# Optimization experiments

Hardware: AMD Instinct MI355X
Metric: run time of the kernel (lower is better)

Reference implementation:

```python
import jax, jax.numpy as jnp
import numpy as np

N_NODES = 50000
N_EDGES = 640000
HID = 128
EDGE_FEAT = 4
NUM_G = 20
R_MIN, R_MAX = 0.0, 10.0

def setup_inputs() -> dict:
    key = jax.random.key(0)
    ks = jax.random.split(key, 16)
    s = lambda d: 1.0 / np.sqrt(d)
    return {
        'h': jax.random.normal(ks[0], (N_NODES, HID), jnp.float32),
        'x': jax.random.normal(ks[1], (N_NODES, 3), jnp.float32),
        'edge_index': jax.random.randint(ks[2], (2, N_EDGES), 0, N_NODES, dtype=jnp.int64),
        'mask_ligand': jnp.ones((N_NODES,), jnp.float32),
        'edge_attr': jax.random.normal(ks[3], (N_EDGES, EDGE_FEAT), jnp.float32),
        'We1': jax.random.normal(ks[4], (2*HID+EDGE_FEAT+NUM_G, HID), jnp.float32) * s(2*HID+EDGE_FEAT+NUM_G),
        'be1': jnp.zeros((HID,), jnp.float32),
        'We2': jax.random.normal(ks[5], (HID, HID), jnp.float32) * s(HID),
        'be2': jnp.zeros((HID,), jnp.float32),
        'Winf': jax.random.normal(ks[6], (HID, 1), jnp.float32) * s(HID),
        'binf': jnp.zeros((1,), jnp.float32),
        'Wx1': jax.random.normal(ks[7], (HID, HID), jnp.float32) * s(HID),
        'bx1': jnp.zeros((HID,), jnp.float32),
        'Wx2': jax.random.normal(ks[8], (HID, 1), jnp.float32) * 0.001 * s(HID),
        'Wn1': jax.random.normal(ks[9], (2*HID, HID), jnp.float32) * s(2*HID),
        'bn1': jnp.zeros((HID,), jnp.float32),
        'Wn2': jax.random.normal(ks[10], (HID, HID), jnp.float32) * s(HID),
        'bn2': jnp.zeros((HID,), jnp.float32),
    }

def reference(h, x, edge_index, mask_ligand, edge_attr,
              We1, be1, We2, be2, Winf, binf, Wx1, bx1, Wx2, Wn1, bn1, Wn2, bn2):
    n = h.shape[0]
    src, dst = edge_index[0], edge_index[1]
    hi, hj = h[dst], h[src]                      # [E, H] gathers
    rel_x = x[dst] - x[src]                      # [E, 3]
    d_sq = jnp.sum(rel_x**2, axis=-1, keepdims=True)  # [E, 1]
    d = jnp.sqrt(d_sq + 1e-8)
    # GaussianSmearing(r_min=0, r_max=10, num_gaussians=20)
    offset = jnp.linspace(R_MIN, R_MAX, NUM_G, dtype=h.dtype)
    coeff = -0.5 / (offset[1] - offset[0])**2
    d_feat = jnp.exp(coeff * (d - offset)**2)    # [E, 20]
    edge_feat = jnp.concatenate([d_feat, edge_attr], axis=-1)
    # edge MLP (2 layers, silu, act_last=True)
    z = jnp.concatenate([hi, hj, edge_feat], axis=-1)
    mij = jax.nn.silu(jax.nn.silu(z @ We1 + be1) @ We2 + be2)  # [E, H]
    eij = jax.nn.sigmoid(mij @ Winf + binf)      # [E, 1]
    mi = jax.ops.segment_sum(mij * eij, dst, num_segments=n)   # [N, H]
    # node MLP (2 layers, silu, no act on last)
    nz = jnp.concatenate([mi, h], axis=-1)
    h_out = h + (jax.nn.silu(nz @ Wn1 + bn1) @ Wn2 + bn2)
    # coordinate update
    xg = jnp.tanh(jax.nn.silu(mij @ Wx1 + bx1) @ Wx2)          # [E, 1]
    delta_x = jax.ops.segment_sum(rel_x / (d + 1.0) * xg, dst, num_segments=n)
    x_out = x + delta_x * mask_ligand[:, None]
    return h_out, x_out
```

## Files before the change

### kernel.cpp

```cpp
#include <hip/hip_runtime.h>
#include <math.h>

#define NN 50000
#define NE 640000
#define H 128
#define EPB 32
#define NPB 32
#define ZB 296
#define BB 136
#define KP1 288
#define NZB 264

typedef __attribute__((ext_vector_type(8))) unsigned short u16x8;
typedef __attribute__((ext_vector_type(8))) __bf16 bf16x8;
typedef __attribute__((ext_vector_type(2))) __bf16 bf16x2;
typedef __attribute__((ext_vector_type(4))) float f32x4;

__device__ __forceinline__ float frcp(float x) {
#if __has_builtin(__builtin_amdgcn_rcpf)
    return __builtin_amdgcn_rcpf(x);
#else
    return 1.0f / x;
#endif
}

__device__ __forceinline__ float silu_f(float v) {
    return v * frcp(1.0f + __expf(-v));
}

__device__ __forceinline__ float sigmoid_f(float v) {
    return frcp(1.0f + __expf(-v));
}

__device__ __forceinline__ float tanh_f(float v) {
    return 1.0f - 2.0f * frcp(1.0f + __expf(2.0f * v));
}

__device__ __forceinline__ unsigned short f2bf(float f) {
    unsigned int u = __builtin_bit_cast(unsigned int, f);
    u += 0x7FFFu + ((u >> 16) & 1u);
    return (unsigned short)(u >> 16);
}

__device__ __forceinline__ float bf2f(unsigned short s) {
    unsigned int u = ((unsigned int)s) << 16;
    return __builtin_bit_cast(float, u);
}

__device__ __forceinline__ unsigned int pkbf(float lo, float hi) {
#if __has_builtin(__builtin_amdgcn_cvt_pk_bf16_f32)
    bf16x2 v = __builtin_amdgcn_cvt_pk_bf16_f32(lo, hi);
    unsigned int r; __builtin_memcpy(&r, &v, 4); return r;
#else
    return (unsigned int)f2bf(lo) | ((unsigned int)f2bf(hi) << 16);
#endif
}

__device__ __forceinline__ f32x4 mfma16(u16x8 a, u16x8 b, f32x4 c) {
    return __builtin_amdgcn_mfma_f32_16x16x32_bf16(
        __builtin_bit_cast(bf16x8, a), __builtin_bit_cast(bf16x8, b), c, 0, 0, 0);
}

template<int KT, int INSTR, bool SYNC_BEFORE_EPI>
__device__ __forceinline__ void layer_mfma(
    const unsigned short* __restrict__ inbuf,
    const unsigned short* __restrict__ wt,
    const float* __restrict__ bias,
    unsigned short* __restrict__ outbuf,
    int wv, int quad, int r16)
{
    f32x4 acc[2][2] = {};
    const int F = wv * 32;
    #pragma unroll
    for (int ks = 0; ks < KT / 32; ks++) {
        int ko = ks * 32 + quad * 8;
        u16x8 b0 = *(const u16x8*)(inbuf + r16 * INSTR + ko);
        u16x8 b1 = *(const u16x8*)(inbuf + (16 + r16) * INSTR + ko);
        u16x8 a0 = *(const u16x8*)(wt + (size_t)(F + r16) * KT + ko);
        u16x8 a1 = *(const u16x8*)(wt + (size_t)(F + 16 + r16) * KT + ko);
        acc[0][0] = mfma16(a0, b0, acc[0][0]);
        acc[0][1] = mfma16(a0, b1, acc[0][1]);
        acc[1][0] = mfma16(a1, b0, acc[1][0]);
        acc[1][1] = mfma16(a1, b1, acc[1][1]);
    }
    if (SYNC_BEFORE_EPI) __syncthreads();
    #pragma unroll
    for (int rt = 0; rt < 2; rt++) {
        int f0 = F + rt * 16 + quad * 4;
        float4 bv = *(const float4*)(bias + f0);
        #pragma unroll
        for (int ci = 0; ci < 2; ci++) {
            int e = ci * 16 + r16;
            float s0 = silu_f(acc[rt][ci][0] + bv.x);
            float s1 = silu_f(acc[rt][ci][1] + bv.y);
            float s2 = silu_f(acc[rt][ci][2] + bv.z);
            float s3 = silu_f(acc[rt][ci][3] + bv.w);
            uint2 p = { pkbf(s0, s1), pkbf(s2, s3) };
            *(uint2*)(outbuf + e * BB + f0) = p;
        }
    }
}

__global__ __launch_bounds__(256) void convert_weights(
    const float* __restrict__ We1, const float* __restrict__ We2,
    const float* __restrict__ Wx1, const float* __restrict__ Wn1,
    const float* __restrict__ Wn2,
    unsigned short* __restrict__ w1t, unsigned short* __restrict__ w2t,
    unsigned short* __restrict__ wx1t, unsigned short* __restrict__ wn1t,
    unsigned short* __restrict__ wn2t)
{
    int i = blockIdx.x * 256 + threadIdx.x;
    const int S1 = 128 * KP1;
    const int S2 = 128 * 128;
    const int S3 = 128 * 256;
    if (i < S1) {
        int n = i / KP1, k = i % KP1;
        w1t[i] = (k < 280) ? f2bf(We1[k * H + n]) : (unsigned short)0;
    } else if (i < S1 + S2) {
        int j = i - S1; int n = j / H, k = j % H;
        w2t[j] = f2bf(We2[k * H + n]);
    } else if (i < S1 + 2 * S2) {
        int j = i - S1 - S2; int n = j / H, k = j % H;
        wx1t[j] = f2bf(Wx1[k * H + n]);
    } else if (i < S1 + 2 * S2 + S3) {
        int j = i - S1 - 2 * S2; int n = j / 256, k = j % 256;
        wn1t[j] = f2bf(Wn1[k * H + n]);
    } else if (i < S1 + 3 * S2 + S3) {
        int j = i - S1 - 2 * S2 - S3; int n = j / H, k = j % H;
        wn2t[j] = f2bf(Wn2[k * H + n]);
    }
}

__global__ __launch_bounds__(256) void zero_kernel(float4* __restrict__ p, int n4) {
    int i = blockIdx.x * 256 + threadIdx.x;
    if (i < n4) p[i] = make_float4(0.f, 0.f, 0.f, 0.f);
}

__global__ __launch_bounds__(256, 7) void edge_kernel(
    const float* __restrict__ h, const float* __restrict__ x,
    const int* __restrict__ ei, const float* __restrict__ edge_attr,
    const unsigned short* __restrict__ w1t, const float* __restrict__ be1,
    const unsigned short* __restrict__ w2t, const float* __restrict__ be2,
    const float* __restrict__ Winf, const float* __restrict__ binf,
    const unsigned short* __restrict__ wx1t, const float* __restrict__ bx1,
    const float* __restrict__ Wx2,
    float* __restrict__ mi, float* __restrict__ dx)
{
    __shared__ unsigned short zs[EPB * ZB];
    __shared__ float relx_s[EPB][3];
    __shared__ float eij_s[EPB];
    __shared__ float epart[4][EPB];
    __shared__ float xpart[4][EPB];
    __shared__ int dst_s[EPB];
    __shared__ float winf_s[H];
    __shared__ float wx2_s[H];

    unsigned short* m1 = zs;
    unsigned short* m2 = zs + EPB * BB;

    const int t = threadIdx.x;
    const int e0 = blockIdx.x * EPB;

    if (t >= 128 && t < 256) {
        winf_s[t - 128] = Winf[t - 128];
        wx2_s[t - 128] = Wx2[t - 128];
    }

    {
        int e = t >> 3, l = t & 7;
        int s = ei[e0 + e], d = ei[NE + e0 + e];
        const float4* hd = (const float4*)(h + (size_t)d * H);
        const float4* hs = (const float4*)(h + (size_t)s * H);
        unsigned short* zr = zs + e * ZB;
        float4 v0 = hd[l * 4 + 0], v1 = hd[l * 4 + 1];
        float4 v2 = hd[l * 4 + 2], v3 = hd[l * 4 + 3];
        uint4 p0 = { pkbf(v0.x, v0.y), pkbf(v0.z, v0.w), pkbf(v1.x, v1.y), pkbf(v1.z, v1.w) };
        uint4 p1 = { pkbf(v2.x, v2.y), pkbf(v2.z, v2.w), pkbf(v3.x, v3.y), pkbf(v3.z, v3.w) };
        *(uint4*)(zr + l * 16) = p0;
        *(uint4*)(zr + l * 16 + 8) = p1;
        float4 w0 = hs[l * 4 + 0], w1 = hs[l * 4 + 1];
        float4 w2 = hs[l * 4 + 2], w3 = hs[l * 4 + 3];
        uint4 q0 = { pkbf(w0.x, w0.y), pkbf(w0.z, w0.w), pkbf(w1.x, w1.y), pkbf(w1.z, w1.w) };
        uint4 q1 = { pkbf(w2.x, w2.y), pkbf(w2.z, w2.w), pkbf(w3.x, w3.y), pkbf(w3.z, w3.w) };
        *(uint4*)(zr + 128 + l * 16) = q0;
        *(uint4*)(zr + 128 + l * 16 + 8) = q1;
    }
    if (t < EPB) {
        int s = ei[e0 + t], d = ei[NE + e0 + t];
        dst_s[t] = d;
        float rx = x[d * 3 + 0] - x[s * 3 + 0];
        float ry = x[d * 3 + 1] - x[s * 3 + 1];
        float rz = x[d * 3 + 2] - x[s * 3 + 2];
        float d2 = rx * rx + ry * ry + rz * rz;
        float dd = sqrtf(d2 + 1e-8f);
        float inv = frcp(dd + 1.0f);
        relx_s[t][0] = rx * inv;
        relx_s[t][1] = ry * inv;
        relx_s[t][2] = rz * inv;
        const float step = 10.0f / 19.0f;
        const float coeff = -0.5f / (step * step);
        unsigned short* zr = zs + t * ZB;
        #pragma unroll
        for (int g = 0; g < 20; g++) {
            float df = dd - step * (float)g;
            zr[256 + g] = f2bf(__expf(coeff * df * df));
        }
        #pragma unroll
        for (int j = 0; j < 4; j++)
            zr[276 + j] = f2bf(edge_attr[(size_t)(e0 + t) * 4 + j]);
        #pragma unroll
        for (int j = 280; j < ZB; j++) zr[j] = 0;
    }
    __syncthreads();

    const int wv = t >> 6, lane = t & 63;
    const int quad = lane >> 4, r16 = lane & 15;
    const int F = wv * 32;

    layer_mfma<KP1, ZB, true>(zs, w1t, be1, m1, wv, quad, r16);
    __syncthreads();

    {
        f32x4 acc[2][2] = {};
        #pragma unroll
        for (int ks = 0; ks < H / 32; ks++) {
            int ko = ks * 32 + quad * 8;
            u16x8 b0 = *(const u16x8*)(m1 + r16 * BB + ko);
            u16x8 b1 = *(const u16x8*)(m1 + (16 + r16) * BB + ko);
            u16x8 a0 = *(const u16x8*)(w2t + (size_t)(F + r16) * H + ko);
            u16x8 a1 = *(const u16x8*)(w2t + (size_t)(F + 16 + r16) * H + ko);
            acc[0][0] = mfma16(a0, b0, acc[0][0]);
            acc[0][1] = mfma16(a0, b1, acc[0][1]);
            acc[1][0] = mfma16(a1, b0, acc[1][0]);
            acc[1][1] = mfma16(a1, b1, acc[1][1]);
        }
        float ep[2] = {0.f, 0.f};
        #pragma unroll
        for (int rt = 0; rt < 2; rt++) {
            int f0 = F + rt * 16 + quad * 4;
            float4 bv = *(const float4*)(be2 + f0);
            float4 wf = *(const float4*)(winf_s + f0);
            #pragma unroll
            for (int ci = 0; ci < 2; ci++) {
                int e = ci * 16 + r16;
                float s0 = silu_f(acc[rt][ci][0] + bv.x);
                float s1 = silu_f(acc[rt][ci][1] + bv.y);
                float s2 = silu_f(acc[rt][ci][2] + bv.z);
                float s3 = silu_f(acc[rt][ci][3] + bv.w);
                ep[ci] += s0 * wf.x + s1 * wf.y + s2 * wf.z + s3 * wf.w;
                uint2 p = { pkbf(s0, s1), pkbf(s2, s3) };
                *(uint2*)(m2 + e * BB + f0) = p;
            }
        }
        #pragma unroll
        for (int ci = 0; ci < 2; ci++) {
            ep[ci] += __shfl_xor(ep[ci], 16, 64);
            ep[ci] += __shfl_xor(ep[ci], 32, 64);
        }
        if (quad == 0) {
            epart[wv][r16] = ep[0];
            epart[wv][16 + r16] = ep[1];
        }
    }
    __syncthreads();

    if (t < EPB) {
        float s = epart[0][t] + epart[1][t] + epart[2][t] + epart[3][t] + binf[0];
        eij_s[t] = sigmoid_f(s);
    }

    {
        f32x4 acc[2][2] = {};
        #pragma unroll
        for (int ks = 0; ks < H / 32; ks++) {
            int ko = ks * 32 + quad * 8;
            u16x8 b0 = *(const u16x8*)(m2 + r16 * BB + ko);
            u16x8 b1 = *(const u16x8*)(m2 + (16 + r16) * BB + ko);
            u16x8 a0 = *(const u16x8*)(wx1t + (size_t)(F + r16) * H + ko);
            u16x8 a1 = *(const u16x8*)(wx1t + (size_t)(F + 16 + r16) * H + ko);
            acc[0][0] = mfma16(a0, b0, acc[0][0]);
            acc[0][1] = mfma16(a0, b1, acc[0][1]);
            acc[1][0] = mfma16(a1, b0, acc[1][0]);
            acc[1][1] = mfma16(a1, b1, acc[1][1]);
        }
        float xp[2] = {0.f, 0.f};
        #pragma unroll
        for (int rt = 0; rt < 2; rt++) {
            int f0 = F + rt * 16 + quad * 4;
            float4 bv = *(const float4*)(bx1 + f0);
            float4 wf = *(const float4*)(wx2_s + f0);
            #pragma unroll
            for (int ci = 0; ci < 2; ci++) {
                xp[ci] += silu_f(acc[rt][ci][0] + bv.x) * wf.x
                        + silu_f(acc[rt][ci][1] + bv.y) * wf.y
                        + silu_f(acc[rt][ci][2] + bv.z) * wf.z
                        + silu_f(acc[rt][ci][3] + bv.w) * wf.w;
            }
        }
        #pragma unroll
        for (int ci = 0; ci < 2; ci++) {
            xp[ci] += __shfl_xor(xp[ci], 16, 64);
            xp[ci] += __shfl_xor(xp[ci], 32, 64);
        }
        if (quad == 0) {
            xpart[wv][r16] = xp[0];
            xpart[wv][16 + r16] = xp[1];
        }
    }
    __syncthreads();

    {
        int k = t & 127, eh = t >> 7;
        for (int e = eh; e < EPB; e += 2) {
            float mv = bf2f(m2[e * BB + k]) * eij_s[e];
            atomicAdd(&mi[(size_t)dst_s[e] * H + k], mv);
        }
        if (t < EPB * 3) {
            int e = t / 3, dim = t % 3;
            float xs = xpart[0][e] + xpart[1][e] + xpart[2][e] + xpart[3][e];
            float xg = tanh_f(xs);
            atomicAdd(&dx[(size_t)dst_s[e] * 3 + dim], relx_s[e][dim] * xg);
        }
    }
}

__global__ __launch_bounds__(256, 8) void node_kernel(
    const float* __restrict__ h, const float* __restrict__ x,
    const float* __restrict__ mask,
    const unsigned short* __restrict__ wn1t, const float* __restrict__ bn1,
    const unsigned short* __restrict__ wn2t, const float* __restrict__ bn2,
    float* __restrict__ mi_hout, float* __restrict__ dx_xout)
{
    __shared__ unsigned short nzs[NPB * NZB];

    unsigned short* nbuf = nzs;

    const int t = threadIdx.x;
    const int n0 = blockIdx.x * NPB;

    {
        int r = t >> 3, l = t & 7;
        int n = n0 + r;
        unsigned short* zr = nzs + r * NZB;
        if (n < NN) {
            const float4* mi4 = (const float4*)(mi_hout + (size_t)n * H);
            const float4* h4  = (const float4*)(h + (size_t)n * H);
            float4 v0 = mi4[l * 4 + 0], v1 = mi4[l * 4 + 1];
            float4 v2 = mi4[l * 4 + 2], v3 = mi4[l * 4 + 3];
            uint4 p0 = { pkbf(v0.x, v0.y), pkbf(v0.z, v0.w), pkbf(v1.x, v1.y), pkbf(v1.z, v1.w) };
            uint4 p1 = { pkbf(v2.x, v2.y), pkbf(v2.z, v2.w), pkbf(v3.x, v3.y), pkbf(v3.z, v3.w) };
            *(uint4*)(zr + l * 16) = p0;
            *(uint4*)(zr + l * 16 + 8) = p1;
            float4 w0 = h4[l * 4 + 0], w1 = h4[l * 4 + 1];
            float4 w2 = h4[l * 4 + 2], w3 = h4[l * 4 + 3];
            uint4 q0 = { pkbf(w0.x, w0.y), pkbf(w0.z, w0.w), pkbf(w1.x, w1.y), pkbf(w1.z, w1.w) };
            uint4 q1 = { pkbf(w2.x, w2.y), pkbf(w2.z, w2.w), pkbf(w3.x, w3.y), pkbf(w3.z, w3.w) };
            *(uint4*)(zr + 128 + l * 16) = q0;
            *(uint4*)(zr + 128 + l * 16 + 8) = q1;
        } else {
            uint4 zf = {0u, 0u, 0u, 0u};
            *(uint4*)(zr + l * 16) = zf;
            *(uint4*)(zr + l * 16 + 8) = zf;
            *(uint4*)(zr + 128 + l * 16) = zf;
            *(uint4*)(zr + 128 + l * 16 + 8) = zf;
        }
    }

    float xo = 0.f;
    int xn = -1, xdim = 0;
    if (t < NPB * 3) {
        int r = t / 3; xdim = t % 3;
        int n = n0 + r;
        if (n < NN) {
            xn = n;
            xo = x[(size_t)n * 3 + xdim] + dx_xout[(size_t)n * 3 + xdim] * mask[n];
        }
    }
    __syncthreads();

    if (xn >= 0) dx_xout[(size_t)xn * 3 + xdim] = xo;

    const int wv = t >> 6, lane = t & 63;
    const int quad = lane >> 4, r16 = lane & 15;

    layer_mfma<2 * H, NZB, true>(nzs, wn1t, bn1, nbuf, wv, quad, r16);
    __syncthreads();

    {
        f32x4 acc[2][2] = {};
        const int F = wv * 32;
        #pragma unroll
        for (int ks = 0; ks < H / 32; ks++) {
            int ko = ks * 32 + quad * 8;
            u16x8 b0 = *(const u16x8*)(nbuf + r16 * BB + ko);
            u16x8 b1 = *(const u16x8*)(nbuf + (16 + r16) * BB + ko);
            u16x8 a0 = *(const u16x8*)(wn2t + (size_t)(F + r16) * H + ko);
            u16x8 a1 = *(const u16x8*)(wn2t + (size_t)(F + 16 + r16) * H + ko);
            acc[0][0] = mfma16(a0, b0, acc[0][0]);
            acc[0][1] = mfma16(a0, b1, acc[0][1]);
            acc[1][0] = mfma16(a1, b0, acc[1][0]);
            acc[1][1] = mfma16(a1, b1, acc[1][1]);
        }
        #pragma unroll
        for (int rt = 0; rt < 2; rt++) {
            int f0 = F + rt * 16 + quad * 4;
            float4 bv = *(const float4*)(bn2 + f0);
            #pragma unroll
            for (int ci = 0; ci < 2; ci++) {
                int n = n0 + ci * 16 + r16;
                if (n < NN) {
                    float4 hv = *(const float4*)(h + (size_t)n * H + f0);
                    float4 o;
                    o.x = hv.x + acc[rt][ci][0] + bv.x;
                    o.y = hv.y + acc[rt][ci][1] + bv.y;
                    o.z = hv.z + acc[rt][ci][2] + bv.z;
                    o.w = hv.w + acc[rt][ci][3] + bv.w;
                    *(float4*)(mi_hout + (size_t)n * H + f0) = o;
                }
            }
        }
    }
}

extern "C" void kernel_launch(void* const* d_in, const int* in_sizes, int n_in,
                              void* d_out, int out_size, void* d_ws, size_t ws_size,
                              hipStream_t stream) {
    const float* h     = (const float*)d_in[0];
    const float* x     = (const float*)d_in[1];
    const int*   ei    = (const int*)d_in[2];
    const float* mask  = (const float*)d_in[3];
    const float* eattr = (const float*)d_in[4];
    const float* We1   = (const float*)d_in[5];
    const float* be1   = (const float*)d_in[6];
    const float* We2   = (const float*)d_in[7];
    const float* be2   = (const float*)d_in[8];
    const float* Winf  = (const float*)d_in[9];
    const float* binf  = (const float*)d_in[10];
    const float* Wx1   = (const float*)d_in[11];
    const float* bx1   = (const float*)d_in[12];
    const float* Wx2   = (const float*)d_in[13];
    const float* Wn1   = (const float*)d_in[14];
    const float* bn1   = (const float*)d_in[15];
    const float* Wn2   = (const float*)d_in[16];
    const float* bn2   = (const float*)d_in[17];

    float* mi = (float*)d_out;
    float* dx = mi + (size_t)NN * H;

    unsigned short* w1t  = (unsigned short*)d_ws;
    unsigned short* w2t  = w1t + 128 * KP1;
    unsigned short* wx1t = w2t + 128 * H;
    unsigned short* wn1t = wx1t + 128 * H;
    unsigned short* wn2t = wn1t + 128 * 256;

    const int wconv_total = 128 * KP1 + 3 * 128 * H + 128 * 256;
    convert_weights<<<(wconv_total + 255) / 256, 256, 0, stream>>>(
        We1, We2, Wx1, Wn1, Wn2, w1t, w2t, wx1t, wn1t, wn2t);

    const int total4 = (NN * H + NN * 3) / 4;
    zero_kernel<<<(total4 + 255) / 256, 256, 0, stream>>>((float4*)d_out, total4);

    edge_kernel<<<NE / EPB, 256, 0, stream>>>(
        h, x, ei, eattr, w1t, be1, w2t, be2, Winf, binf, wx1t, bx1, Wx2, mi, dx);

    node_kernel<<<(NN + NPB - 1) / NPB, 256, 0, stream>>>(
        h, x, mask, wn1t, bn1, wn2t, bn2, mi, dx);
}
```

Measured before the change: 525.9 us.

## Sort edges by destination via counting sort and segment-reduce before atomics

After: 558.6 us. 6.2% more time.

```diff
diff --git a/kernel.cpp b/kernel.cpp
--- a/kernel.cpp
+++ b/kernel.cpp
@@ -10,6 +10,7 @@
 #define BB 136
 #define KP1 288
 #define NZB 264
+#define NBPAD 50176
 
 typedef __attribute__((ext_vector_type(8))) unsigned short u16x8;
 typedef __attribute__((ext_vector_type(8))) __bf16 bf16x8;
@@ -136,6 +137,48 @@
     if (i < n4) p[i] = make_float4(0.f, 0.f, 0.f, 0.f);
 }
 
+__global__ __launch_bounds__(256) void hist_kernel(
+    const int* __restrict__ ei, int* __restrict__ cnt)
+{
+    int i = blockIdx.x * 256 + threadIdx.x;
+    if (i < NE) atomicAdd(&cnt[ei[NE + i]], 1);
+}
+
+__global__ __launch_bounds__(256) void scan_kernel(
+    const int* __restrict__ cnt, int* __restrict__ cur)
+{
+    __shared__ int part[256];
+    const int t = threadIdx.x;
+    const int lo = t * (NBPAD / 256);
+    int s = 0;
+    for (int i = 0; i < NBPAD / 256; i++) s += cnt[lo + i];
+    part[t] = s;
+    __syncthreads();
+    #pragma unroll
+    for (int d = 1; d < 256; d <<= 1) {
+        int v = (t >= d) ? part[t - d] : 0;
+        __syncthreads();
+        part[t] += v;
+        __syncthreads();
+    }
+    int run = (t > 0) ? part[t - 1] : 0;
+    for (int i = 0; i < NBPAD / 256; i++) {
+        cur[lo + i] = run;
+        run += cnt[lo + i];
+    }
+}
+
+__global__ __launch_bounds__(256) void scatter_kernel(
+    const int* __restrict__ ei, int* __restrict__ cur, int* __restrict__ perm)
+{
+    int i = blockIdx.x * 256 + threadIdx.x;
+    if (i < NE) {
+        int d = ei[NE + i];
+        int p = atomicAdd(&cur[d], 1);
+        perm[p] = i;
+    }
+}
+
 __global__ __launch_bounds__(256, 7) void edge_kernel(
     const float* __restrict__ h, const float* __restrict__ x,
     const int* __restrict__ ei, const float* __restrict__ edge_attr,
@@ -143,7 +186,7 @@
     const unsigned short* __restrict__ w2t, const float* __restrict__ be2,
     const float* __restrict__ Winf, const float* __restrict__ binf,
     const unsigned short* __restrict__ wx1t, const float* __restrict__ bx1,
-    const float* __restrict__ Wx2,
+    const float* __restrict__ Wx2, const int* __restrict__ perm,
     float* __restrict__ mi, float* __restrict__ dx)
 {
     __shared__ unsigned short zs[EPB * ZB];
@@ -160,6 +203,7 @@
 
     const int t = threadIdx.x;
     const int e0 = blockIdx.x * EPB;
+    const bool srt = (perm != nullptr);
 
     if (t >= 128 && t < 256) {
         winf_s[t - 128] = Winf[t - 128];
@@ -168,7 +212,8 @@
 
     {
         int e = t >> 3, l = t & 7;
-        int s = ei[e0 + e], d = ei[NE + e0 + e];
+        int ep = srt ? perm[e0 + e] : (e0 + e);
+        int s = ei[ep], d = ei[NE + ep];
         const float4* hd = (const float4*)(h + (size_t)d * H);
         const float4* hs = (const float4*)(h + (size_t)s * H);
         unsigned short* zr = zs + e * ZB;
@@ -186,7 +231,8 @@
         *(uint4*)(zr + 128 + l * 16 + 8) = q1;
     }
     if (t < EPB) {
-        int s = ei[e0 + t], d = ei[NE + e0 + t];
+        int ep = srt ? perm[e0 + t] : (e0 + t);
+        int s = ei[ep], d = ei[NE + ep];
         dst_s[t] = d;
         float rx = x[d * 3 + 0] - x[s * 3 + 0];
         float ry = x[d * 3 + 1] - x[s * 3 + 1];
@@ -207,7 +253,7 @@
         }
         #pragma unroll
         for (int j = 0; j < 4; j++)
-            zr[276 + j] = f2bf(edge_attr[(size_t)(e0 + t) * 4 + j]);
+            zr[276 + j] = f2bf(edge_attr[(size_t)ep * 4 + j]);
         #pragma unroll
         for (int j = 280; j < ZB; j++) zr[j] = 0;
     }
@@ -310,16 +356,33 @@
     __syncthreads();
 
     {
-        int k = t & 127, eh = t >> 7;
-        for (int e = eh; e < EPB; e += 2) {
-            float mv = bf2f(m2[e * BB + k]) * eij_s[e];
-            atomicAdd(&mi[(size_t)dst_s[e] * H + k], mv);
-        }
-        if (t < EPB * 3) {
-            int e = t / 3, dim = t % 3;
-            float xs = xpart[0][e] + xpart[1][e] + xpart[2][e] + xpart[3][e];
-            float xg = tanh_f(xs);
-            atomicAdd(&dx[(size_t)dst_s[e] * 3 + dim], relx_s[e][dim] * xg);
+        if (t < 128) {
+            const int k = t;
+            float acc = 0.f;
+            int rs = 0;
+            #pragma unroll 1
+            for (int e = 0; e < EPB; e++) {
+                acc += bf2f(m2[e * BB + k]) * eij_s[e];
+                if (e == EPB - 1 || dst_s[e + 1] != dst_s[e]) {
+                    float* p = &mi[(size_t)dst_s[e] * H + k];
+                    if (srt && rs > 0 && e < EPB - 1) *p = acc;
+                    else atomicAdd(p, acc);
+                    acc = 0.f;
+                    rs = e + 1;
+                }
+            }
+        } else if (t < 131) {
+            const int dd = t - 128;
+            float acc = 0.f;
+            #pragma unroll 1
+            for (int e = 0; e < EPB; e++) {
+                float xs = xpart[0][e] + xpart[1][e] + xpart[2][e] + xpart[3][e];
+                acc += relx_s[e][dd] * tanh_f(xs);
+                if (e == EPB - 1 || dst_s[e + 1] != dst_s[e]) {
+                    atomicAdd(&dx[(size_t)dst_s[e] * 3 + dd], acc);
+                    acc = 0.f;
+                }
+            }
         }
     }
 }
@@ -453,6 +516,13 @@
     unsigned short* wn1t = wx1t + 128 * H;
     unsigned short* wn2t = wn1t + 128 * 256;
 
+    char* wsb  = (char*)d_ws;
+    int*  cnt  = (int*)(wsb + (256 << 10));
+    int*  cur  = cnt + NBPAD;
+    int*  perm = cur + NBPAD;
+    const size_t ws_needed = (size_t)(256 << 10) + (size_t)(2 * NBPAD + NE) * sizeof(int);
+    const bool do_sort = (ws_size >= ws_needed);
+
     const int wconv_total = 128 * KP1 + 3 * 128 * H + 128 * 256;
     convert_weights<<<(wconv_total + 255) / 256, 256, 0, stream>>>(
         We1, We2, Wx1, Wn1, Wn2, w1t, w2t, wx1t, wn1t, wn2t);
@@ -460,8 +530,16 @@
     const int total4 = (NN * H + NN * 3) / 4;
     zero_kernel<<<(total4 + 255) / 256, 256, 0, stream>>>((float4*)d_out, total4);
 
+    if (do_sort) {
+        zero_kernel<<<(NBPAD / 4 + 255) / 256, 256, 0, stream>>>((float4*)cnt, NBPAD / 4);
+        hist_kernel<<<(NE + 255) / 256, 256, 0, stream>>>(ei, cnt);
+        scan_kernel<<<1, 256, 0, stream>>>(cnt, cur);
+        scatter_kernel<<<(NE + 255) / 256, 256, 0, stream>>>(ei, cur, perm);
+    }
+
     edge_kernel<<<NE / EPB, 256, 0, stream>>>(
-        h, x, ei, eattr, w1t, be1, w2t, be2, Winf, binf, wx1t, bx1, Wx2, mi, dx);
+        h, x, ei, eattr, w1t, be1, w2t, be2, Winf, binf, wx1t, bx1, Wx2,
+        do_sort ? perm : (const int*)nullptr, mi, dx);
 
     node_kernel<<<(NN + NPB - 1) / NPB, 256, 0, stream>>>(
         h, x, mask, wn1t, bn1, wn2t, bn2, mi, dx);
```
